# Kernel optimization log

Hardware: AMD Instinct MI355X
Metric: run time of the kernel (lower is better)

Reference implementation:

```python
import jax, jax.numpy as jnp
import numpy as np

B, S, D = 4, 4096, 1024          # batch, seq, d_model
K, H, A = 32, 4, 2               # mem_key_dim, mem_hashes, mem_assoc
T, NB = 65536, 16                # mem_buckets = 2**NB
Dm, Tv = 64, 32                  # mem_dim, mem_vsa_dim
READ_TEMP, VSA_W = 1.0, 1.0
TANH_SCALE, BETA, NOV_THR = 1.0, 1.0, 0.0
WRITE_THR, ETA = 0.5, 0.1


def setup_inputs() -> dict:
    key = jax.random.key(0)
    k = jax.random.split(key, 12)
    s = 0.02
    return {
        "u": jax.random.normal(k[0], (B, S, D), jnp.float32),
        "Wq": jax.random.normal(k[1], (K, D), jnp.float32) * s,
        "Ww": jax.random.normal(k[2], (K, D), jnp.float32) * s,
        "Wv": jax.random.normal(k[3], (Dm, D), jnp.float32) * s,
        "Wout": jax.random.normal(k[4], (D, Dm), jnp.float32) * s,
        "Wg": jax.random.normal(k[5], (1, D), jnp.float32) * s,
        "bg": jnp.zeros((1,), jnp.float32),
        "R": jax.random.normal(k[6], (H, K, NB), jnp.float32),
        "P": jax.random.normal(k[7], (Tv, K), jnp.float32) / np.float32(np.sqrt(K)),
        "mem_keys": jax.random.normal(k[8], (T, A, K), jnp.float32),
        "mem_vals": jax.random.normal(k[9], (T, A, Dm), jnp.float32),
        "mem_tags": jnp.tanh(jax.random.normal(k[10], (T, A, Tv), jnp.float32)),
    }


def reference(u, Wq, Ww, Wv, Wout, Wg, bg, R, P, mem_keys, mem_vals, mem_tags):
    # --- routing (BitRouter): sign bits of random projections -> bucket per hash ---
    q = jnp.einsum('bsd,kd->bsk', u, Wq)                              # query tag
    bits = (jnp.einsum('bsk,hkn->bshn', q, R) > 0).astype(jnp.int32)
    pw = 2 ** jnp.arange(NB, dtype=jnp.int32)
    idx = jnp.sum(bits * pw, axis=-1)                                 # [B,S,H] in [0,T)

    # --- read: gather bucket slots, key + VSA-tag scores, softmax over H*A ---
    Kg, Vg, Tg = mem_keys[idx], mem_vals[idx], mem_tags[idx]          # [B,S,H,A,*]
    score = jnp.einsum('bsk,bshak->bsha', q, Kg) / jnp.sqrt(jnp.float32(K))
    qt = jnp.tanh(TANH_SCALE * jnp.einsum('bsk,tk->bst', q, P))       # VSA tag of query
    score = score + VSA_W * jnp.einsum('bst,bshat->bsha', qt, Tg) / Tv
    attn = jax.nn.softmax((score / READ_TEMP).reshape(B, S, H * A), axis=-1)
    attn = attn.reshape(B, S, H, A)
    read = jnp.einsum('bsha,bshad->bsd', attn, Vg)                    # [B,S,Dm]
    y = jnp.einsum('bsm,dm->bsd', read, Wout)                         # [B,S,D]

    # --- write: gate + VSA novelty, blend best-matching slot, scatter-add ---
    wk = jnp.einsum('bsd,kd->bsk', u, Ww)
    v = jnp.einsum('bsd,md->bsm', u, Wv)
    g = jax.nn.sigmoid(jnp.einsum('bsd,od->bso', u, Wg) + bg)[..., 0]  # [B,S]
    wt = jnp.tanh(TANH_SCALE * jnp.einsum('bsk,tk->bst', wk, P))
    match = jnp.einsum('bst,bshat->bsha', wt, Tg) / Tv
    slot = jnp.argmax(match, axis=-1)                                  # [B,S,H]
    nov = jax.nn.sigmoid(BETA * (NOV_THR - jnp.max(match, axis=-1)))   # novelty gate
    w = ETA * (g * (g > WRITE_THR))[..., None] * nov                   # [B,S,H]
    flat = (idx * A + slot).reshape(-1)                                # [B*S*H]

    def blend(table, gathered, target, dim):
        cur = jnp.take_along_axis(gathered, slot[..., None, None], axis=3)[..., 0, :]
        d = (w[..., None] * (target[:, :, None, :] - cur)).reshape(-1, dim)
        return table.reshape(T * A, dim).at[flat].add(d).reshape(T, A, dim)

    new_keys = blend(mem_keys, Kg, wk, K)
    new_vals = blend(mem_vals, Vg, v, Dm)
    new_tags = blend(mem_tags, Tg, wt, Tv)
    return y, new_keys, new_vals, new_tags
```

## Files before the change

### kernel.cpp

```cpp
#include <hip/hip_runtime.h>
#include <hip/hip_bf16.h>
#include <cstdint>

#define BB 4
#define SS 4096
#define DD 1024
#define KK 32
#define HH 4
#define AA 2
#define TT 65536
#define NBB 16
#define DM 64
#define TV 32
#define MTOK (BB*SS)
#define PKS 4
#define PKL (DD/PKS)

#define WAVE_FENCE() asm volatile("s_waitcnt lgkmcnt(0)" ::: "memory")

__global__ __launch_bounds__(256, 2) void proj_kernel(
    const float* __restrict__ u, const float* __restrict__ Wq,
    const float* __restrict__ Ww, const float* __restrict__ Wv,
    const float* __restrict__ Wg,
    float* __restrict__ qs, float* __restrict__ wks,
    float* __restrict__ vs, float* __restrict__ gs)
{
    __shared__ float u_t[128][36];
    __shared__ float w_t[128][36];
    const int t  = threadIdx.x;
    const int mb = blockIdx.x & 127;
    const int ks = blockIdx.x >> 7;
    const int m0 = mb * 128;
    const int kb = ks * PKL;
    const int r0 = t >> 3;
    const int c8 = t & 7;
    const int ty = t >> 4;
    const int tx = t & 15;

    float acc[8][8];
#pragma unroll
    for (int i = 0; i < 8; i++)
#pragma unroll
        for (int j = 0; j < 8; j++) acc[i][j] = 0.f;
    float gp[4] = {0.f, 0.f, 0.f, 0.f};

    for (int k0 = 0; k0 < PKL; k0 += 32) {
        const float4 wg4 = *(const float4*)(Wg + kb + k0 + c8 * 4);
        __syncthreads();
#pragma unroll
        for (int p = 0; p < 4; p++) {
            int r = r0 + 32 * p;
            float4 uv = *(const float4*)(u + (size_t)(m0 + r) * DD + kb + k0 + c8 * 4);
            *(float4*)&u_t[r][c8 * 4] = uv;
            gp[p] = fmaf(uv.x, wg4.x, fmaf(uv.y, wg4.y, fmaf(uv.z, wg4.z, fmaf(uv.w, wg4.w, gp[p]))));
        }
#pragma unroll
        for (int p = 0; p < 4; p++) {
            int c = r0 + 32 * p;
            const float* wrow = (c < 32)  ? (Wq + (size_t)c * DD)
                              : (c < 64)  ? (Ww + (size_t)(c - 32) * DD)
                                          : (Wv + (size_t)(c - 64) * DD);
            *(float4*)&w_t[c][c8 * 4] = *(const float4*)(wrow + kb + k0 + c8 * 4);
        }
        __syncthreads();
#pragma unroll
        for (int k4 = 0; k4 < 8; k4++) {
            float4 a4[8], b4[8];
#pragma unroll
            for (int i = 0; i < 8; i++) a4[i] = *(const float4*)&u_t[ty + 16 * i][k4 * 4];
#pragma unroll
            for (int j = 0; j < 8; j++) b4[j] = *(const float4*)&w_t[tx + 16 * j][k4 * 4];
#pragma unroll
            for (int i = 0; i < 8; i++)
#pragma unroll
                for (int j = 0; j < 8; j++) {
                    acc[i][j] = fmaf(a4[i].x, b4[j].x, acc[i][j]);
                    acc[i][j] = fmaf(a4[i].y, b4[j].y, acc[i][j]);
                    acc[i][j] = fmaf(a4[i].z, b4[j].z, acc[i][j]);
                    acc[i][j] = fmaf(a4[i].w, b4[j].w, acc[i][j]);
                }
        }
    }
#pragma unroll
    for (int p = 0; p < 4; p++) {
        gp[p] += __shfl_xor(gp[p], 1);
        gp[p] += __shfl_xor(gp[p], 2);
        gp[p] += __shfl_xor(gp[p], 4);
    }
    if (c8 == 0) {
#pragma unroll
        for (int p = 0; p < 4; p++) gs[(size_t)ks * MTOK + m0 + r0 + 32 * p] = gp[p];
    }
#pragma unroll
    for (int i = 0; i < 8; i++) {
        int row = m0 + ty + 16 * i;
#pragma unroll
        for (int j = 0; j < 8; j++) {
            if (j < 2)      qs[(size_t)ks * MTOK * KK + (size_t)row * KK + tx + 16 * j]        = acc[i][j];
            else if (j < 4) wks[(size_t)ks * MTOK * KK + (size_t)row * KK + tx + 16 * (j - 2)] = acc[i][j];
            else            vs[(size_t)ks * MTOK * DM + (size_t)row * DM + tx + 16 * (j - 4)]  = acc[i][j];
        }
    }
}

__global__ __launch_bounds__(256) void route_kernel(
    const float* __restrict__ R, const float* __restrict__ P,
    const float* __restrict__ mem_keys, const float* __restrict__ mem_vals,
    const float* __restrict__ mem_tags, const float* __restrict__ bg,
    const float* __restrict__ qs, const float* __restrict__ wks,
    const float* __restrict__ gsl,
    float* __restrict__ read_o, float* __restrict__ wt_o,
    int* __restrict__ idx_o, int* __restrict__ slot_o, float* __restrict__ w_o)
{
    __shared__ float R_s[4 * 528];
    __shared__ float P_s[TV][KK + 1];
    __shared__ float q_s[4][KK], wk_s[4][KK], qt_s[4][TV], wt_s[4][TV];
    __shared__ float kg_s[4][8][KK], tg_s[4][8][TV], vg_s[4][8][DM];
    __shared__ float sc_s[4][8], mt_s[4][8];
    __shared__ int   idx_s[4][HH];

    const int t    = threadIdx.x;
    const int wid  = t >> 6;
    const int lane = t & 63;

    for (int e = t; e < 2048; e += 256) R_s[(e >> 9) * 528 + (e & 511)] = R[e];
    for (int e = t; e < TV * KK; e += 256) P_s[e >> 5][e & 31] = P[e];
    const float bgv = bg[0];
    __syncthreads();

    for (int ti = 0; ti < 4; ti++) {
        const int tok = blockIdx.x * 16 + wid * 4 + ti;
        if (lane < 32) {
            float s = 0.f;
#pragma unroll
            for (int sl = 0; sl < PKS; sl++) s += qs[(size_t)sl * MTOK * KK + (size_t)tok * KK + lane];
            q_s[wid][lane] = s;
        } else {
            int l2 = lane - 32;
            float s = 0.f;
#pragma unroll
            for (int sl = 0; sl < PKS; sl++) s += wks[(size_t)sl * MTOK * KK + (size_t)tok * KK + l2];
            wk_s[wid][l2] = s;
        }
        WAVE_FENCE();
        {
            int h = lane >> 4, n = lane & 15;
            float s = 0.f;
#pragma unroll
            for (int k = 0; k < KK; k++) s = fmaf(q_s[wid][k], R_s[h * 528 + k * 16 + n], s);
            unsigned long long m = __ballot(s > 0.f);
            if (n == 0) {
                int idx = (int)((m >> (h * 16)) & 0xFFFFull);
                idx_s[wid][h] = idx;
                idx_o[(size_t)tok * HH + h] = idx;
            }
        }
        if (lane < 32) {
            float s = 0.f;
#pragma unroll
            for (int k = 0; k < KK; k++) s = fmaf(q_s[wid][k], P_s[lane][k], s);
            qt_s[wid][lane] = tanhf(s);
        } else {
            int t2 = lane - 32;
            float s = 0.f;
#pragma unroll
            for (int k = 0; k < KK; k++) s = fmaf(wk_s[wid][k], P_s[t2][k], s);
            float wtv = tanhf(s);
            wt_s[wid][t2] = wtv;
            wt_o[(size_t)tok * TV + t2] = wtv;
        }
        WAVE_FENCE();
        {
            int p = lane >> 3, j = lane & 7;
            int h = p >> 1, a = p & 1;
            size_t sb = (size_t)idx_s[wid][h] * AA + a;
            *(float4*)&kg_s[wid][p][j * 4] = *(const float4*)(mem_keys + sb * KK + j * 4);
            *(float4*)&tg_s[wid][p][j * 4] = *(const float4*)(mem_tags + sb * TV + j * 4);
            *(float4*)&vg_s[wid][p][j * 8]     = *(const float4*)(mem_vals + sb * DM + j * 8);
            *(float4*)&vg_s[wid][p][j * 8 + 4] = *(const float4*)(mem_vals + sb * DM + j * 8 + 4);
        }
        WAVE_FENCE();
        if (lane < 8) {
            int p = lane;
            float s1 = 0.f, s2 = 0.f;
#pragma unroll
            for (int k = 0; k < KK; k++) s1 = fmaf(q_s[wid][k], kg_s[wid][p][k], s1);
#pragma unroll
            for (int k = 0; k < TV; k++) s2 = fmaf(qt_s[wid][k], tg_s[wid][p][k], s2);
            sc_s[wid][p] = s1 * 0.17677669529663688f + s2 * (1.0f / 32.0f);
        } else if (lane < 16) {
            int p = lane - 8;
            float s2 = 0.f;
#pragma unroll
            for (int k = 0; k < TV; k++) s2 = fmaf(wt_s[wid][k], tg_s[wid][p][k], s2);
            mt_s[wid][p] = s2 * (1.0f / 32.0f);
        }
        WAVE_FENCE();
        {
            float sc[8];
#pragma unroll
            for (int p = 0; p < 8; p++) sc[p] = sc_s[wid][p];
            float mx = sc[0];
#pragma unroll
            for (int p = 1; p < 8; p++) mx = fmaxf(mx, sc[p]);
            float e[8], den = 0.f;
#pragma unroll
            for (int p = 0; p < 8; p++) { e[p] = expf(sc[p] - mx); den += e[p]; }
            float inv = 1.f / den;
            float r = 0.f;
#pragma unroll
            for (int p = 0; p < 8; p++) r = fmaf(e[p] * inv, vg_s[wid][p][lane], r);
            read_o[(size_t)tok * DM + lane] = r;
        }
        if (lane < HH) {
            int h = lane;
            float m0v = mt_s[wid][h * 2], m1v = mt_s[wid][h * 2 + 1];
            int sl = (m1v > m0v) ? 1 : 0;
            float mm = fmaxf(m0v, m1v);
            float nov = 1.f / (1.f + expf(mm));
            float gd = bgv;
#pragma unroll
            for (int s2 = 0; s2 < PKS; s2++) gd += gsl[(size_t)s2 * MTOK + tok];
            float gg = 1.f / (1.f + expf(-gd));
            float wv = (gg > 0.5f) ? (0.1f * gg * nov) : 0.f;
            slot_o[(size_t)tok * HH + h] = sl;
            w_o[(size_t)tok * HH + h] = wv;
        }
        WAVE_FENCE();
    }
}

__global__ __launch_bounds__(256) void ygemm_kernel(
    const float* __restrict__ read_i, const float* __restrict__ Wout,
    float* __restrict__ y_o)
{
    __shared__ float rd_t[64][68];
    __shared__ float wo_t[64][68];
    const int t  = threadIdx.x;
    const int m0 = blockIdx.x * 64;
    const int n0 = blockIdx.y * 64;
#pragma unroll
    for (int i = 0; i < 4; i++) {
        int e = t + i * 256;
        int r = e >> 4, cv = e & 15;
        *(float4*)&rd_t[r][cv * 4] = *(const float4*)(read_i + (size_t)(m0 + r) * DM + cv * 4);
        *(float4*)&wo_t[r][cv * 4] = *(const float4*)(Wout  + (size_t)(n0 + r) * DM + cv * 4);
    }
    __syncthreads();
    const int ty = t >> 4;
    const int tx = t & 15;
    float acc[4][4];
#pragma unroll
    for (int i = 0; i < 4; i++)
#pragma unroll
        for (int j = 0; j < 4; j++) acc[i][j] = 0.f;
#pragma unroll
    for (int k4 = 0; k4 < 16; k4++) {
        float4 a4[4], b4[4];
#pragma unroll
        for (int i = 0; i < 4; i++) a4[i] = *(const float4*)&rd_t[ty * 4 + i][k4 * 4];
#pragma unroll
        for (int j = 0; j < 4; j++) b4[j] = *(const float4*)&wo_t[tx + j * 16][k4 * 4];
#pragma unroll
        for (int i = 0; i < 4; i++)
#pragma unroll
            for (int j = 0; j < 4; j++) {
                acc[i][j] = fmaf(a4[i].x, b4[j].x, acc[i][j]);
                acc[i][j] = fmaf(a4[i].y, b4[j].y, acc[i][j]);
                acc[i][j] = fmaf(a4[i].z, b4[j].z, acc[i][j]);
                acc[i][j] = fmaf(a4[i].w, b4[j].w, acc[i][j]);
            }
    }
#pragma unroll
    for (int i = 0; i < 4; i++) {
        size_t row = (size_t)(m0 + ty * 4 + i) * DD + n0;
#pragma unroll
        for (int j = 0; j < 4; j++) y_o[row + tx + j * 16] = acc[i][j];
    }
}

__global__ __launch_bounds__(256) void scatter_kernel(
    const float* __restrict__ mem_keys, const float* __restrict__ mem_vals,
    const float* __restrict__ mem_tags,
    const float* __restrict__ wks, const float* __restrict__ vsl,
    const float* __restrict__ wt_i,
    const int* __restrict__ idx_i, const int* __restrict__ slot_i,
    const float* __restrict__ w_i,
    float* __restrict__ keys_o, float* __restrict__ vals_o, float* __restrict__ tags_o)
{
    int op   = blockIdx.x * 8 + (threadIdx.x >> 5);
    int lane = threadIdx.x & 31;
    float w = w_i[op];
    if (w == 0.f) return;
    int tok = op >> 2;
    size_t flat = (size_t)idx_i[op] * AA + slot_i[op];
    {
        float wkv = 0.f;
#pragma unroll
        for (int sl = 0; sl < PKS; sl++) wkv += wks[(size_t)sl * MTOK * KK + (size_t)tok * KK + lane];
        float d = w * (wkv - mem_keys[flat * KK + lane]);
        atomicAdd(keys_o + flat * KK + lane, d);
    }
    {
        float d = w * (wt_i[(size_t)tok * TV + lane] - mem_tags[flat * TV + lane]);
        atomicAdd(tags_o + flat * TV + lane, d);
    }
#pragma unroll
    for (int h2 = 0; h2 < 2; h2++) {
        int d2 = lane + h2 * 32;
        float vv = 0.f;
#pragma unroll
        for (int sl = 0; sl < PKS; sl++) vv += vsl[(size_t)sl * MTOK * DM + (size_t)tok * DM + d2];
        float d = w * (vv - mem_vals[flat * DM + d2]);
        atomicAdd(vals_o + flat * DM + d2, d);
    }
}

extern "C" void kernel_launch(void* const* d_in, const int* in_sizes, int n_in,
                              void* d_out, int out_size, void* d_ws, size_t ws_size,
                              hipStream_t stream)
{
    (void)in_sizes; (void)n_in; (void)out_size; (void)ws_size;
    const float* u    = (const float*)d_in[0];
    const float* Wq   = (const float*)d_in[1];
    const float* Ww   = (const float*)d_in[2];
    const float* Wv   = (const float*)d_in[3];
    const float* Wout = (const float*)d_in[4];
    const float* Wg   = (const float*)d_in[5];
    const float* bg   = (const float*)d_in[6];
    const float* R    = (const float*)d_in[7];
    const float* P    = (const float*)d_in[8];
    const float* mem_keys = (const float*)d_in[9];
    const float* mem_vals = (const float*)d_in[10];
    const float* mem_tags = (const float*)d_in[11];

    float* y_o    = (float*)d_out;
    float* keys_o = y_o    + (size_t)MTOK * DD;
    float* vals_o = keys_o + (size_t)TT * AA * KK;
    float* tags_o = vals_o + (size_t)TT * AA * DM;

    float* qs  = y_o;
    float* wks = qs  + (size_t)PKS * MTOK * KK;
    float* vsl = wks + (size_t)PKS * MTOK * KK;
    float* gsl = vsl + (size_t)PKS * MTOK * DM;

    float* ws     = (float*)d_ws;
    float* read_w = ws;
    float* wt_w   = read_w + (size_t)MTOK * DM;
    float* w_w    = wt_w   + (size_t)MTOK * TV;
    int*   idx_w  = (int*)(w_w + (size_t)MTOK * HH);
    int*   slot_w = idx_w + (size_t)MTOK * HH;

    hipMemcpyAsync(keys_o, mem_keys, (size_t)TT * AA * KK * sizeof(float), hipMemcpyDeviceToDevice, stream);
    hipMemcpyAsync(vals_o, mem_vals, (size_t)TT * AA * DM * sizeof(float), hipMemcpyDeviceToDevice, stream);
    hipMemcpyAsync(tags_o, mem_tags, (size_t)TT * AA * TV * sizeof(float), hipMemcpyDeviceToDevice, stream);

    proj_kernel<<<128 * PKS, 256, 0, stream>>>(u, Wq, Ww, Wv, Wg, qs, wks, vsl, gsl);
    route_kernel<<<MTOK / 16, 256, 0, stream>>>(R, P, mem_keys, mem_vals, mem_tags, bg,
                                                qs, wks, gsl, read_w, wt_w, idx_w, slot_w, w_w);
    scatter_kernel<<<MTOK * HH / 8, 256, 0, stream>>>(mem_keys, mem_vals, mem_tags,
        wks, vsl, wt_w, idx_w, slot_w, w_w, keys_o, vals_o, tags_o);
    ygemm_kernel<<<dim3(MTOK / 64, DD / 64), 256, 0, stream>>>(read_w, Wout, y_o);
}
```

Measured before the change: 370.9 us.

## Fuse scatter into route kernel, merge table copies, enlarge y-GEMM tiles

Moves the write/scatter-add step into the routing kernel, reusing the gathered key/tag/value rows and wk/wt already held in shared memory. This removes the separate scatter kernel and the workspace round trips for idx, slot, w and wt. The three device-to-device memcpys are replaced by one grid-stride copy kernel, and the output GEMM moves from 64x64 to 128x128 tiles with an 8x8 register block. In exchange, the route kernel carries more work and register pressure, and the larger GEMM tile lowers block count.

After: 369.9 us. No clear change (-0.3%).

```diff
diff --git a/kernel.cpp b/kernel.cpp
--- a/kernel.cpp
+++ b/kernel.cpp
@@ -18,6 +18,26 @@
 
 #define WAVE_FENCE() asm volatile("s_waitcnt lgkmcnt(0)" ::: "memory")
 
+__global__ __launch_bounds__(256) void copy_kernel(
+    const float* __restrict__ mem_keys, const float* __restrict__ mem_vals,
+    const float* __restrict__ mem_tags, float* __restrict__ tab_o)
+{
+    const size_t NK = (size_t)TT * AA * KK;
+    const size_t NV = (size_t)TT * AA * DM;
+    const size_t NT = (size_t)TT * AA * TV;
+    const size_t total4 = (NK + NV + NT) / 4;
+    size_t i = (size_t)blockIdx.x * 256 + threadIdx.x;
+    const size_t stride = (size_t)gridDim.x * 256;
+    for (; i < total4; i += stride) {
+        size_t e = i * 4;
+        float4 val;
+        if (e < NK)           val = *(const float4*)(mem_keys + e);
+        else if (e < NK + NV) val = *(const float4*)(mem_vals + (e - NK));
+        else                  val = *(const float4*)(mem_tags + (e - NK - NV));
+        *(float4*)(tab_o + e) = val;
+    }
+}
+
 __global__ __launch_bounds__(256, 2) void proj_kernel(
     const float* __restrict__ u, const float* __restrict__ Wq,
     const float* __restrict__ Ww, const float* __restrict__ Wv,
@@ -108,16 +128,17 @@
     const float* __restrict__ mem_keys, const float* __restrict__ mem_vals,
     const float* __restrict__ mem_tags, const float* __restrict__ bg,
     const float* __restrict__ qs, const float* __restrict__ wks,
-    const float* __restrict__ gsl,
-    float* __restrict__ read_o, float* __restrict__ wt_o,
-    int* __restrict__ idx_o, int* __restrict__ slot_o, float* __restrict__ w_o)
+    const float* __restrict__ vsl, const float* __restrict__ gsl,
+    float* __restrict__ read_o,
+    float* __restrict__ keys_o, float* __restrict__ vals_o, float* __restrict__ tags_o)
 {
     __shared__ float R_s[4 * 528];
     __shared__ float P_s[TV][KK + 1];
     __shared__ float q_s[4][KK], wk_s[4][KK], qt_s[4][TV], wt_s[4][TV];
     __shared__ float kg_s[4][8][KK], tg_s[4][8][TV], vg_s[4][8][DM];
     __shared__ float sc_s[4][8], mt_s[4][8];
-    __shared__ int   idx_s[4][HH];
+    __shared__ float w_s[4][HH];
+    __shared__ int   idx_s[4][HH], slot_s[4][HH];
 
     const int t    = threadIdx.x;
     const int wid  = t >> 6;
@@ -149,11 +170,7 @@
 #pragma unroll
             for (int k = 0; k < KK; k++) s = fmaf(q_s[wid][k], R_s[h * 528 + k * 16 + n], s);
             unsigned long long m = __ballot(s > 0.f);
-            if (n == 0) {
-                int idx = (int)((m >> (h * 16)) & 0xFFFFull);
-                idx_s[wid][h] = idx;
-                idx_o[(size_t)tok * HH + h] = idx;
-            }
+            if (n == 0) idx_s[wid][h] = (int)((m >> (h * 16)) & 0xFFFFull);
         }
         if (lane < 32) {
             float s = 0.f;
@@ -165,9 +182,7 @@
             float s = 0.f;
 #pragma unroll
             for (int k = 0; k < KK; k++) s = fmaf(wk_s[wid][k], P_s[t2][k], s);
-            float wtv = tanhf(s);
-            wt_s[wid][t2] = wtv;
-            wt_o[(size_t)tok * TV + t2] = wtv;
+            wt_s[wid][t2] = tanhf(s);
         }
         WAVE_FENCE();
         {
@@ -223,96 +238,88 @@
             for (int s2 = 0; s2 < PKS; s2++) gd += gsl[(size_t)s2 * MTOK + tok];
             float gg = 1.f / (1.f + expf(-gd));
             float wv = (gg > 0.5f) ? (0.1f * gg * nov) : 0.f;
-            slot_o[(size_t)tok * HH + h] = sl;
-            w_o[(size_t)tok * HH + h] = wv;
-        }
-        WAVE_FENCE();
-    }
-}
-
-__global__ __launch_bounds__(256) void ygemm_kernel(
+            slot_s[wid][h] = sl;
+            w_s[wid][h] = wv;
+        }
+        WAVE_FENCE();
+        if (w_s[wid][0] != 0.f) {
+            float vsum = 0.f;
+#pragma unroll
+            for (int sl = 0; sl < PKS; sl++) vsum += vsl[(size_t)sl * MTOK * DM + (size_t)tok * DM + lane];
+            int h = lane >> 4, c = lane & 15;
+            float wv = w_s[wid][h];
+            int sl8 = slot_s[wid][h];
+            size_t flat = (size_t)idx_s[wid][h] * AA + sl8;
+            int p = h * 2 + sl8;
+#pragma unroll
+            for (int m = 0; m < 2; m++) {
+                int cc = c + 16 * m;
+                atomicAdd(keys_o + flat * KK + cc, wv * (wk_s[wid][cc] - kg_s[wid][p][cc]));
+                atomicAdd(tags_o + flat * TV + cc, wv * (wt_s[wid][cc] - tg_s[wid][p][cc]));
+            }
+#pragma unroll
+            for (int m = 0; m < 4; m++) {
+                int cc = c + 16 * m;
+                float vv = __shfl(vsum, cc);
+                atomicAdd(vals_o + flat * DM + cc, wv * (vv - vg_s[wid][p][cc]));
+            }
+        }
+        WAVE_FENCE();
+    }
+}
+
+__global__ __launch_bounds__(256, 2) void ygemm_kernel(
     const float* __restrict__ read_i, const float* __restrict__ Wout,
     float* __restrict__ y_o)
 {
-    __shared__ float rd_t[64][68];
-    __shared__ float wo_t[64][68];
+    __shared__ float rd_t[128][36];
+    __shared__ float wo_t[128][36];
     const int t  = threadIdx.x;
-    const int m0 = blockIdx.x * 64;
-    const int n0 = blockIdx.y * 64;
-#pragma unroll
-    for (int i = 0; i < 4; i++) {
-        int e = t + i * 256;
-        int r = e >> 4, cv = e & 15;
-        *(float4*)&rd_t[r][cv * 4] = *(const float4*)(read_i + (size_t)(m0 + r) * DM + cv * 4);
-        *(float4*)&wo_t[r][cv * 4] = *(const float4*)(Wout  + (size_t)(n0 + r) * DM + cv * 4);
-    }
-    __syncthreads();
+    const int m0 = blockIdx.x * 128;
+    const int n0 = blockIdx.y * 128;
+    const int r0 = t >> 3;
+    const int c8 = t & 7;
     const int ty = t >> 4;
     const int tx = t & 15;
-    float acc[4][4];
-#pragma unroll
-    for (int i = 0; i < 4; i++)
-#pragma unroll
-        for (int j = 0; j < 4; j++) acc[i][j] = 0.f;
-#pragma unroll
-    for (int k4 = 0; k4 < 16; k4++) {
-        float4 a4[4], b4[4];
-#pragma unroll
-        for (int i = 0; i < 4; i++) a4[i] = *(const float4*)&rd_t[ty * 4 + i][k4 * 4];
-#pragma unroll
-        for (int j = 0; j < 4; j++) b4[j] = *(const float4*)&wo_t[tx + j * 16][k4 * 4];
-#pragma unroll
-        for (int i = 0; i < 4; i++)
-#pragma unroll
-            for (int j = 0; j < 4; j++) {
-                acc[i][j] = fmaf(a4[i].x, b4[j].x, acc[i][j]);
-                acc[i][j] = fmaf(a4[i].y, b4[j].y, acc[i][j]);
-                acc[i][j] = fmaf(a4[i].z, b4[j].z, acc[i][j]);
-                acc[i][j] = fmaf(a4[i].w, b4[j].w, acc[i][j]);
-            }
-    }
-#pragma unroll
-    for (int i = 0; i < 4; i++) {
-        size_t row = (size_t)(m0 + ty * 4 + i) * DD + n0;
-#pragma unroll
-        for (int j = 0; j < 4; j++) y_o[row + tx + j * 16] = acc[i][j];
-    }
-}
-
-__global__ __launch_bounds__(256) void scatter_kernel(
-    const float* __restrict__ mem_keys, const float* __restrict__ mem_vals,
-    const float* __restrict__ mem_tags,
-    const float* __restrict__ wks, const float* __restrict__ vsl,
-    const float* __restrict__ wt_i,
-    const int* __restrict__ idx_i, const int* __restrict__ slot_i,
-    const float* __restrict__ w_i,
-    float* __restrict__ keys_o, float* __restrict__ vals_o, float* __restrict__ tags_o)
-{
-    int op   = blockIdx.x * 8 + (threadIdx.x >> 5);
-    int lane = threadIdx.x & 31;
-    float w = w_i[op];
-    if (w == 0.f) return;
-    int tok = op >> 2;
-    size_t flat = (size_t)idx_i[op] * AA + slot_i[op];
-    {
-        float wkv = 0.f;
-#pragma unroll
-        for (int sl = 0; sl < PKS; sl++) wkv += wks[(size_t)sl * MTOK * KK + (size_t)tok * KK + lane];
-        float d = w * (wkv - mem_keys[flat * KK + lane]);
-        atomicAdd(keys_o + flat * KK + lane, d);
-    }
-    {
-        float d = w * (wt_i[(size_t)tok * TV + lane] - mem_tags[flat * TV + lane]);
-        atomicAdd(tags_o + flat * TV + lane, d);
-    }
-#pragma unroll
-    for (int h2 = 0; h2 < 2; h2++) {
-        int d2 = lane + h2 * 32;
-        float vv = 0.f;
-#pragma unroll
-        for (int sl = 0; sl < PKS; sl++) vv += vsl[(size_t)sl * MTOK * DM + (size_t)tok * DM + d2];
-        float d = w * (vv - mem_vals[flat * DM + d2]);
-        atomicAdd(vals_o + flat * DM + d2, d);
+
+    float acc[8][8];
+#pragma unroll
+    for (int i = 0; i < 8; i++)
+#pragma unroll
+        for (int j = 0; j < 8; j++) acc[i][j] = 0.f;
+
+    for (int k0 = 0; k0 < DM; k0 += 32) {
+        __syncthreads();
+#pragma unroll
+        for (int p = 0; p < 4; p++) {
+            int r = r0 + 32 * p;
+            *(float4*)&rd_t[r][c8 * 4] = *(const float4*)(read_i + (size_t)(m0 + r) * DM + k0 + c8 * 4);
+            *(float4*)&wo_t[r][c8 * 4] = *(const float4*)(Wout  + (size_t)(n0 + r) * DM + k0 + c8 * 4);
+        }
+        __syncthreads();
+#pragma unroll
+        for (int k4 = 0; k4 < 8; k4++) {
+            float4 a4[8], b4[8];
+#pragma unroll
+            for (int i = 0; i < 8; i++) a4[i] = *(const float4*)&rd_t[ty + 16 * i][k4 * 4];
+#pragma unroll
+            for (int j = 0; j < 8; j++) b4[j] = *(const float4*)&wo_t[tx + 16 * j][k4 * 4];
+#pragma unroll
+            for (int i = 0; i < 8; i++)
+#pragma unroll
+                for (int j = 0; j < 8; j++) {
+                    acc[i][j] = fmaf(a4[i].x, b4[j].x, acc[i][j]);
+                    acc[i][j] = fmaf(a4[i].y, b4[j].y, acc[i][j]);
+                    acc[i][j] = fmaf(a4[i].z, b4[j].z, acc[i][j]);
+                    acc[i][j] = fmaf(a4[i].w, b4[j].w, acc[i][j]);
+                }
+        }
+    }
+#pragma unroll
+    for (int i = 0; i < 8; i++) {
+        size_t row = (size_t)(m0 + ty + 16 * i) * DD + n0;
+#pragma unroll
+        for (int j = 0; j < 8; j++) y_o[row + tx + 16 * j] = acc[i][j];
     }
 }
 
@@ -344,21 +351,12 @@
     float* vsl = wks + (size_t)PKS * MTOK * KK;
     float* gsl = vsl + (size_t)PKS * MTOK * DM;
 
-    float* ws     = (float*)d_ws;
-    float* read_w = ws;
-    float* wt_w   = read_w + (size_t)MTOK * DM;
-    float* w_w    = wt_w   + (size_t)MTOK * TV;
-    int*   idx_w  = (int*)(w_w + (size_t)MTOK * HH);
-    int*   slot_w = idx_w + (size_t)MTOK * HH;
-
-    hipMemcpyAsync(keys_o, mem_keys, (size_t)TT * AA * KK * sizeof(float), hipMemcpyDeviceToDevice, stream);
-    hipMemcpyAsync(vals_o, mem_vals, (size_t)TT * AA * DM * sizeof(float), hipMemcpyDeviceToDevice, stream);
-    hipMemcpyAsync(tags_o, mem_tags, (size_t)TT * AA * TV * sizeof(float), hipMemcpyDeviceToDevice, stream);
-
+    float* read_w = (float*)d_ws;
+
+    copy_kernel<<<2048, 256, 0, stream>>>(mem_keys, mem_vals, mem_tags, keys_o);
     proj_kernel<<<128 * PKS, 256, 0, stream>>>(u, Wq, Ww, Wv, Wg, qs, wks, vsl, gsl);
     route_kernel<<<MTOK / 16, 256, 0, stream>>>(R, P, mem_keys, mem_vals, mem_tags, bg,
-                                                qs, wks, gsl, read_w, wt_w, idx_w, slot_w, w_w);
-    scatter_kernel<<<MTOK * HH / 8, 256, 0, stream>>>(mem_keys, mem_vals, mem_tags,
-        wks, vsl, wt_w, idx_w, slot_w, w_w, keys_o, vals_o, tags_o);
-    ygemm_kernel<<<dim3(MTOK / 64, DD / 64), 256, 0, stream>>>(read_w, Wout, y_o);
-}
+                                                qs, wks, vsl, gsl, read_w,
+                                                keys_o, vals_o, tags_o);
+    ygemm_kernel<<<dim3(MTOK / 128, DD / 128), 256, 0, stream>>>(read_w, Wout, y_o);
+}
```
